# Performance work log

Measured on AMD Instinct MI355X. Metric: run time of the kernel, lower is better.

Reference implementation:

```python
import jax, jax.numpy as jnp
import numpy as np

E = 8          # num_experts
K = 2          # top-k experts per token
CAP_RATIO = 1.05


def setup_inputs() -> dict:
    key = jax.random.key(0)
    ks = jax.random.split(key, 4)
    B, S, D, H = 2, 2048, 1024, 4096
    x = jax.random.normal(ks[0], (B, S, D), jnp.float32)
    Wg = jax.random.normal(ks[1], (E, D), jnp.float32) * 0.02
    W1 = jax.random.normal(ks[2], (E, D, H), jnp.float32) * 0.02
    b1 = jnp.zeros((E, H), jnp.float32)
    W2 = jax.random.normal(ks[3], (E, H, D), jnp.float32) * 0.02
    b2 = jnp.zeros((E, D), jnp.float32)
    return {"x": x, "Wg": Wg, "W1": W1, "b1": b1, "W2": W2, "b2": b2}


def reference(x, Wg, W1, b1, W2, b2):
    # Eval-mode SparseMoE forward (no router noise, no aux-loss metrics).
    B, S, D = x.shape
    T = B * S
    xf = x.reshape(T, D)

    # --- router: softmax gates + top-k ---
    gates = jax.nn.softmax(xf @ Wg.T, axis=-1)          # [T, E]
    topw, topi = jax.lax.top_k(gates, K)                # [T, K]

    # --- capacity-limited dispatch (slot-major order, matching torch loop) ---
    C = int(round(K * T * CAP_RATIO / E))               # buffer capacity per expert
    e_ord = topi.T.reshape(-1)                          # [K*T] expert id per assignment
    tok_ord = jnp.tile(jnp.arange(T), K)                # [K*T] token id per assignment
    oh = jax.nn.one_hot(e_ord, E, dtype=jnp.int32)      # [K*T, E]
    cnt = jnp.take_along_axis(jnp.cumsum(oh, 0) - oh, e_ord[:, None], 1)[:, 0]
    within = cnt < C                                    # first C arrivals per expert accepted
    pos = jnp.where(within, cnt, C)                     # dropped tokens -> dummy slot C

    # scatter accepted tokens into per-expert buffers [E, C+1, D]
    x_disp = xf[tok_ord]
    buf = jnp.zeros((E, C + 1, D), xf.dtype).at[e_ord, pos].add(x_disp)[:, :C]

    # --- grouped expert MLP (Linear -> exact GELU -> Linear) ---
    h = jax.nn.gelu(jnp.einsum('ecd,edh->ech', buf, W1) + b1[:, None, :],
                    approximate=False)
    y = jnp.einsum('ech,ehd->ecd', h, W2) + b2[:, None, :]  # [E, C, D]

    # --- gather back and weighted combine ---
    y_ord = y[e_ord, jnp.minimum(pos, C - 1)] * within[:, None].astype(y.dtype)
    y_tk = y_ord.reshape(K, T, D).transpose(1, 0, 2)     # [T, K, D]
    cw = topw * within.reshape(K, T).T.astype(topw.dtype)
    out = jnp.einsum('tk,tkd->td', cw, y_tk)
    return out.reshape(B, S, D)
```

## Files before the change

### kernel.cpp

```cpp
#include <hip/hip_runtime.h>

typedef __attribute__((ext_vector_type(8))) __bf16 bf16x8;
typedef __attribute__((ext_vector_type(4))) float f32x4;

constexpr int T  = 4096;
constexpr int Dm = 1024;
constexpr int Hm = 4096;
constexpr int NE = 8;
constexpr int CAP = 1075;
constexpr int CP  = 1152;

static __device__ __forceinline__ unsigned short f2bf(float f) {
  unsigned int u = __float_as_uint(f);
  u += 0x7FFFu + ((u >> 16) & 1u);
  return (unsigned short)(u >> 16);
}

static __device__ __forceinline__ void gload_lds16(const void* g, void* l) {
  __builtin_amdgcn_global_load_lds(
      (const __attribute__((address_space(1))) void*)g,
      (__attribute__((address_space(3))) void*)l, 16, 0, 0);
}

__global__ __launch_bounds__(256) void router_kernel(
    const float* __restrict__ x, const float* __restrict__ Wg,
    int* __restrict__ topi, float* __restrict__ topw) {
  int t = blockIdx.x * 4 + (threadIdx.x >> 6);
  int lane = threadIdx.x & 63;
  const float* xr = x + (size_t)t * Dm;
  float acc[NE];
#pragma unroll
  for (int e = 0; e < NE; ++e) acc[e] = 0.f;
  for (int i = lane * 4; i < Dm; i += 256) {
    float4 xv = *(const float4*)(xr + i);
#pragma unroll
    for (int e = 0; e < NE; ++e) {
      float4 wv = *(const float4*)(Wg + e * Dm + i);
      acc[e] += xv.x * wv.x + xv.y * wv.y + xv.z * wv.z + xv.w * wv.w;
    }
  }
#pragma unroll
  for (int off = 32; off > 0; off >>= 1) {
#pragma unroll
    for (int e = 0; e < NE; ++e) acc[e] += __shfl_xor(acc[e], off, 64);
  }
  if (lane == 0) {
    float mx = acc[0];
#pragma unroll
    for (int e = 1; e < NE; ++e) mx = fmaxf(mx, acc[e]);
    float g[NE];
    float s = 0.f;
#pragma unroll
    for (int e = 0; e < NE; ++e) { g[e] = expf(acc[e] - mx); s += g[e]; }
    int i0 = 0; float v0 = g[0];
#pragma unroll
    for (int e = 1; e < NE; ++e) if (g[e] > v0) { v0 = g[e]; i0 = e; }
    int i1 = -1; float v1 = -1e30f;
#pragma unroll
    for (int e = 0; e < NE; ++e) {
      if (e == i0) continue;
      if (g[e] > v1) { v1 = g[e]; i1 = e; }
    }
    float inv = 1.f / s;
    topi[t * 2] = i0; topi[t * 2 + 1] = i1;
    topw[t * 2] = v0 * inv; topw[t * 2 + 1] = v1 * inv;
  }
}

__global__ void dispatch_kernel(const int* __restrict__ topi,
                                int* __restrict__ pos, int* __restrict__ within) {
  int lane = threadIdx.x;
  int cnt[NE];
#pragma unroll
  for (int e = 0; e < NE; ++e) cnt[e] = 0;
  unsigned long long below = (1ULL << lane) - 1ULL;
  for (int c = 0; c < (2 * T) / 64; ++c) {
    int a = c * 64 + lane;
    int k = a >> 12;
    int t = a & (T - 1);
    int e = topi[t * 2 + k];
    int p = 0;
#pragma unroll
    for (int ex = 0; ex < NE; ++ex) {
      unsigned long long m = __ballot(e == ex);
      if (e == ex) p = cnt[ex] + __popcll(m & below);
      cnt[ex] += __popcll(m);
    }
    pos[a] = p;
    within[a] = (p < CAP) ? 1 : 0;
  }
}

__global__ __launch_bounds__(256) void scatter_kernel(
    const float* __restrict__ x, const int* __restrict__ topi,
    const int* __restrict__ pos, const int* __restrict__ within,
    unsigned short* __restrict__ buf) {
  int a = blockIdx.x;
  if (!within[a]) return;
  int k = a >> 12, t = a & (T - 1);
  int e = topi[t * 2 + k];
  int p = pos[a];
  const float* src = x + (size_t)t * Dm;
  unsigned short* dst = buf + ((size_t)e * CP + p) * Dm;
  int i = threadIdx.x * 4;
  float4 v = *(const float4*)(src + i);
  ushort4 o;
  o.x = f2bf(v.x); o.y = f2bf(v.y); o.z = f2bf(v.z); o.w = f2bf(v.w);
  *(ushort4*)(dst + i) = o;
}

__global__ __launch_bounds__(256) void transpose_kernel(
    const float* __restrict__ W, unsigned short* __restrict__ Wt,
    int Kd, int N) {
  __shared__ float tile[64][33];
  const int e = blockIdx.z;
  const int n0 = blockIdx.x * 32;
  const int k0 = blockIdx.y * 64;
  const float* src = W + ((long long)e * Kd + k0) * N + n0;
  const int tid = threadIdx.x;
  const int r = tid >> 3;
  const int c4 = (tid & 7) * 4;
#pragma unroll
  for (int hh = 0; hh < 2; ++hh) {
    float4 v = *(const float4*)(src + (long long)(r + 32 * hh) * N + c4);
    tile[r + 32 * hh][c4] = v.x; tile[r + 32 * hh][c4 + 1] = v.y;
    tile[r + 32 * hh][c4 + 2] = v.z; tile[r + 32 * hh][c4 + 3] = v.w;
  }
  __syncthreads();
  const int n = tid >> 4;
  const int k4 = (tid & 15) * 4;
  unsigned short* dst = Wt + ((long long)e * N + n0) * Kd + k0;
#pragma unroll
  for (int hh = 0; hh < 2; ++hh) {
    int nn = n + 16 * hh;
    ushort4 o;
    o.x = f2bf(tile[k4][nn]);     o.y = f2bf(tile[k4 + 1][nn]);
    o.z = f2bf(tile[k4 + 2][nn]); o.w = f2bf(tile[k4 + 3][nn]);
    *(ushort4*)(dst + (long long)nn * Kd + k4) = o;
  }
}

template <bool GELU, bool OUT_BF16>
__global__ __launch_bounds__(256) void gemm_bt_kernel(
    const unsigned short* __restrict__ Aall, const unsigned short* __restrict__ Btall,
    const float* __restrict__ biasAll, void* __restrict__ OutAll,
    int Kd, int N, long long sA, long long sB, long long sO, int sBias) {
  __shared__ unsigned short Alds[128 * 64];
  __shared__ unsigned short Blds[128 * 64];

  const int e = blockIdx.z;
  const unsigned short* A  = Aall  + (long long)e * sA + (long long)blockIdx.y * 128 * Kd;
  const unsigned short* Bt = Btall + (long long)e * sB + (long long)blockIdx.x * 128 * Kd;
  const float* bias = biasAll + (long long)e * sBias + blockIdx.x * 128;

  const int tid = threadIdx.x;
  const int lane = tid & 63;
  const int wid = tid >> 6;
  const int wr = (wid >> 1) * 64;
  const int wc = (wid & 1) * 64;
  const int l15 = lane & 15;
  const int khi = lane >> 4;
  const int swz = lane & 7;

  const int srow = lane >> 3;
  const int sslot = (lane & 7) ^ srow;

  f32x4 acc[4][4];
#pragma unroll
  for (int m = 0; m < 4; ++m)
#pragma unroll
    for (int n = 0; n < 4; ++n) acc[m][n] = (f32x4){0.f, 0.f, 0.f, 0.f};

  const int nK = Kd >> 6;
  for (int kt = 0; kt < nK; ++kt) {
    const int kb = kt << 6;
#pragma unroll
    for (int j = 0; j < 4; ++j) {
      const int c = wid * 4 + j;
      const long long rowg = 8 * c + srow;
      gload_lds16(A  + rowg * Kd + kb + sslot * 8, &Alds[c * 512]);
      gload_lds16(Bt + rowg * Kd + kb + sslot * 8, &Blds[c * 512]);
    }
    __syncthreads();
#pragma unroll
    for (int kk = 0; kk < 2; ++kk) {
      bf16x8 af[4], bfv[4];
#pragma unroll
      for (int m = 0; m < 4; ++m)
        af[m] = *(const bf16x8*)&Alds[(wr + m * 16 + l15) * 64 + (((kk * 4 + khi) ^ swz) << 3)];
#pragma unroll
      for (int n = 0; n < 4; ++n)
        bfv[n] = *(const bf16x8*)&Blds[(wc + n * 16 + l15) * 64 + (((kk * 4 + khi) ^ swz) << 3)];
#pragma unroll
      for (int m = 0; m < 4; ++m)
#pragma unroll
        for (int n = 0; n < 4; ++n)
          acc[m][n] = __builtin_amdgcn_mfma_f32_16x16x32_bf16(af[m], bfv[n], acc[m][n], 0, 0, 0);
    }
    __syncthreads();
  }

  const int crow = khi * 4;
#pragma unroll
  for (int m = 0; m < 4; ++m) {
#pragma unroll
    for (int n = 0; n < 4; ++n) {
      const long long col = (long long)blockIdx.x * 128 + wc + n * 16 + l15;
      const float bvv = bias[wc + n * 16 + l15];
#pragma unroll
      for (int j = 0; j < 4; ++j) {
        const long long row = (long long)blockIdx.y * 128 + wr + m * 16 + crow + j;
        float v = acc[m][n][j] + bvv;
        if (GELU) v = 0.5f * v * (1.f + erff(v * 0.70710678118654752f));
        if (OUT_BF16)
          ((unsigned short*)OutAll)[(long long)e * sO + row * N + col] = f2bf(v);
        else
          ((float*)OutAll)[(long long)e * sO + row * N + col] = v;
      }
    }
  }
}

__global__ __launch_bounds__(256) void combine_kernel(
    const float* __restrict__ y, const int* __restrict__ topi,
    const float* __restrict__ topw, const int* __restrict__ pos,
    const int* __restrict__ within, float* __restrict__ out) {
  int t = blockIdx.x;
  int i = threadIdx.x * 4;
  float4 r = {0.f, 0.f, 0.f, 0.f};
#pragma unroll
  for (int k = 0; k < 2; ++k) {
    int a = k * T + t;
    if (within[a]) {
      int e = topi[t * 2 + k];
      int p = pos[a];
      float w = topw[t * 2 + k];
      const float* yr = y + ((size_t)e * CP + p) * Dm;
      float4 v = *(const float4*)(yr + i);
      r.x += w * v.x; r.y += w * v.y; r.z += w * v.z; r.w += w * v.w;
    }
  }
  *(float4*)(out + (size_t)t * Dm + i) = r;
}

extern "C" void kernel_launch(void* const* d_in, const int* in_sizes, int n_in,
                              void* d_out, int out_size, void* d_ws, size_t ws_size,
                              hipStream_t stream) {
  const float* x  = (const float*)d_in[0];
  const float* Wg = (const float*)d_in[1];
  const float* W1 = (const float*)d_in[2];
  const float* b1 = (const float*)d_in[3];
  const float* W2 = (const float*)d_in[4];
  const float* b2 = (const float*)d_in[5];
  float* out = (float*)d_out;

  char* ws = (char*)d_ws;
  const size_t sz_h = (size_t)NE * CP * Hm * 2;
  const size_t sz_y = (size_t)NE * CP * Dm * 4;
  const size_t sz_wt_full = (size_t)NE * Hm * Dm * 2;
  const size_t needA = sz_h + sz_y + sz_wt_full + (size_t)2 * T * 16;
  const int EB = (ws_size >= needA) ? NE : 2;

  unsigned short* h = (unsigned short*)ws;
  char* yreg = ws + sz_h;
  unsigned short* buf = (unsigned short*)yreg;
  float* y = (float*)yreg;
  unsigned short* Wt = (unsigned short*)(ws + sz_h + sz_y);
  char* smallp = ws + sz_h + sz_y + (size_t)EB * Hm * Dm * 2;
  int* topi   = (int*)smallp;
  float* topw = (float*)(topi + 2 * T);
  int* pos    = (int*)(topw + 2 * T);
  int* within = pos + 2 * T;

  router_kernel<<<T / 4, 256, 0, stream>>>(x, Wg, topi, topw);
  dispatch_kernel<<<1, 64, 0, stream>>>(topi, pos, within);
  scatter_kernel<<<2 * T, 256, 0, stream>>>(x, topi, pos, within, buf);

  for (int e0 = 0; e0 < NE; e0 += EB) {
    transpose_kernel<<<dim3(Hm / 32, Dm / 64, EB), 256, 0, stream>>>(
        W1 + (size_t)e0 * Dm * Hm, Wt, Dm, Hm);
    gemm_bt_kernel<true, true><<<dim3(Hm / 128, CP / 128, EB), 256, 0, stream>>>(
        buf + (size_t)e0 * CP * Dm, Wt, b1 + (size_t)e0 * Hm,
        (void*)(h + (size_t)e0 * CP * Hm),
        Dm, Hm, (long long)CP * Dm, (long long)Hm * Dm, (long long)CP * Hm, Hm);
  }
  for (int e0 = 0; e0 < NE; e0 += EB) {
    transpose_kernel<<<dim3(Dm / 32, Hm / 64, EB), 256, 0, stream>>>(
        W2 + (size_t)e0 * Hm * Dm, Wt, Hm, Dm);
    gemm_bt_kernel<false, false><<<dim3(Dm / 128, CP / 128, EB), 256, 0, stream>>>(
        h + (size_t)e0 * CP * Hm, Wt, b2 + (size_t)e0 * Dm,
        (void*)(y + (size_t)e0 * CP * Dm),
        Hm, Dm, (long long)CP * Hm, (long long)Dm * Hm, (long long)CP * Dm, Dm);
  }

  combine_kernel<<<T, 256, 0, stream>>>(y, topi, topw, pos, within, out);
}
```

Measured before the change: 397.6 us.

## Parallelize dispatch with block-wide packed scan and remap GEMM grid to 1D

```diff
diff --git a/kernel.cpp b/kernel.cpp
--- a/kernel.cpp
+++ b/kernel.cpp
@@ -67,25 +67,43 @@
   }
 }
 
-__global__ void dispatch_kernel(const int* __restrict__ topi,
-                                int* __restrict__ pos, int* __restrict__ within) {
-  int lane = threadIdx.x;
-  int cnt[NE];
-#pragma unroll
-  for (int e = 0; e < NE; ++e) cnt[e] = 0;
-  unsigned long long below = (1ULL << lane) - 1ULL;
-  for (int c = 0; c < (2 * T) / 64; ++c) {
-    int a = c * 64 + lane;
+__global__ __launch_bounds__(1024) void dispatch_scan_kernel(
+    const int* __restrict__ topi, int* __restrict__ pos, int* __restrict__ within) {
+  __shared__ unsigned long long sc0[1024];
+  __shared__ unsigned long long sc1[1024];
+  const int tid = threadIdx.x;
+  int myE[8];
+  unsigned long long w0 = 0, w1 = 0;
+#pragma unroll
+  for (int j = 0; j < 8; ++j) {
+    int a = tid * 8 + j;
     int k = a >> 12;
     int t = a & (T - 1);
     int e = topi[t * 2 + k];
-    int p = 0;
-#pragma unroll
-    for (int ex = 0; ex < NE; ++ex) {
-      unsigned long long m = __ballot(e == ex);
-      if (e == ex) p = cnt[ex] + __popcll(m & below);
-      cnt[ex] += __popcll(m);
-    }
+    myE[j] = e;
+    unsigned long long inc = 1ULL << (16 * (e & 3));
+    if (e < 4) w0 += inc; else w1 += inc;
+  }
+  const unsigned long long l0 = w0, l1 = w1;
+  sc0[tid] = w0; sc1[tid] = w1;
+  __syncthreads();
+  for (int off = 1; off < 1024; off <<= 1) {
+    unsigned long long a0 = 0, a1 = 0;
+    if (tid >= off) { a0 = sc0[tid - off]; a1 = sc1[tid - off]; }
+    __syncthreads();
+    w0 += a0; w1 += a1;
+    sc0[tid] = w0; sc1[tid] = w1;
+    __syncthreads();
+  }
+  unsigned long long e0 = w0 - l0, e1 = w1 - l1;
+#pragma unroll
+  for (int j = 0; j < 8; ++j) {
+    int a = tid * 8 + j;
+    int e = myE[j];
+    int sh = 16 * (e & 3);
+    int p;
+    if (e < 4) { p = (int)((e0 >> sh) & 0xFFFF); e0 += 1ULL << sh; }
+    else       { p = (int)((e1 >> sh) & 0xFFFF); e1 += 1ULL << sh; }
     pos[a] = p;
     within[a] = (p < CAP) ? 1 : 0;
   }
@@ -144,14 +162,20 @@
 __global__ __launch_bounds__(256) void gemm_bt_kernel(
     const unsigned short* __restrict__ Aall, const unsigned short* __restrict__ Btall,
     const float* __restrict__ biasAll, void* __restrict__ OutAll,
-    int Kd, int N, long long sA, long long sB, long long sO, int sBias) {
+    int Kd, int N, long long sA, long long sB, long long sO, int sBias,
+    int eb, int nM) {
   __shared__ unsigned short Alds[128 * 64];
   __shared__ unsigned short Blds[128 * 64];
 
-  const int e = blockIdx.z;
-  const unsigned short* A  = Aall  + (long long)e * sA + (long long)blockIdx.y * 128 * Kd;
-  const unsigned short* Bt = Btall + (long long)e * sB + (long long)blockIdx.x * 128 * Kd;
-  const float* bias = biasAll + (long long)e * sBias + blockIdx.x * 128;
+  const int lin = blockIdx.x;
+  const int e = lin % eb;
+  const int q = lin / eb;
+  const int mb = q % nM;
+  const int nb = q / nM;
+
+  const unsigned short* A  = Aall  + (long long)e * sA + (long long)mb * 128 * Kd;
+  const unsigned short* Bt = Btall + (long long)e * sB + (long long)nb * 128 * Kd;
+  const float* bias = biasAll + (long long)e * sBias + nb * 128;
 
   const int tid = threadIdx.x;
   const int lane = tid & 63;
@@ -205,11 +229,11 @@
   for (int m = 0; m < 4; ++m) {
 #pragma unroll
     for (int n = 0; n < 4; ++n) {
-      const long long col = (long long)blockIdx.x * 128 + wc + n * 16 + l15;
+      const long long col = (long long)nb * 128 + wc + n * 16 + l15;
       const float bvv = bias[wc + n * 16 + l15];
 #pragma unroll
       for (int j = 0; j < 4; ++j) {
-        const long long row = (long long)blockIdx.y * 128 + wr + m * 16 + crow + j;
+        const long long row = (long long)mb * 128 + wr + m * 16 + crow + j;
         float v = acc[m][n][j] + bvv;
         if (GELU) v = 0.5f * v * (1.f + erff(v * 0.70710678118654752f));
         if (OUT_BF16)
@@ -273,24 +297,27 @@
   int* within = pos + 2 * T;
 
   router_kernel<<<T / 4, 256, 0, stream>>>(x, Wg, topi, topw);
-  dispatch_kernel<<<1, 64, 0, stream>>>(topi, pos, within);
+  dispatch_scan_kernel<<<1, 1024, 0, stream>>>(topi, pos, within);
   scatter_kernel<<<2 * T, 256, 0, stream>>>(x, topi, pos, within, buf);
 
+  const int nM = CP / 128;
   for (int e0 = 0; e0 < NE; e0 += EB) {
     transpose_kernel<<<dim3(Hm / 32, Dm / 64, EB), 256, 0, stream>>>(
         W1 + (size_t)e0 * Dm * Hm, Wt, Dm, Hm);
-    gemm_bt_kernel<true, true><<<dim3(Hm / 128, CP / 128, EB), 256, 0, stream>>>(
+    gemm_bt_kernel<true, true><<<EB * nM * (Hm / 128), 256, 0, stream>>>(
         buf + (size_t)e0 * CP * Dm, Wt, b1 + (size_t)e0 * Hm,
         (void*)(h + (size_t)e0 * CP * Hm),
-        Dm, Hm, (long long)CP * Dm, (long long)Hm * Dm, (long long)CP * Hm, Hm);
+        Dm, Hm, (long long)CP * Dm, (long long)Hm * Dm, (long long)CP * Hm, Hm,
+        EB, nM);
   }
   for (int e0 = 0; e0 < NE; e0 += EB) {
     transpose_kernel<<<dim3(Dm / 32, Hm / 64, EB), 256, 0, stream>>>(
         W2 + (size_t)e0 * Hm * Dm, Wt, Hm, Dm);
-    gemm_bt_kernel<false, false><<<dim3(Dm / 128, CP / 128, EB), 256, 0, stream>>>(
+    gemm_bt_kernel<false, false><<<EB * nM * (Dm / 128), 256, 0, stream>>>(
         h + (size_t)e0 * CP * Hm, Wt, b2 + (size_t)e0 * Dm,
         (void*)(y + (size_t)e0 * CP * Dm),
-        Hm, Dm, (long long)CP * Hm, (long long)Dm * Hm, (long long)CP * Dm, Dm);
+        Hm, Dm, (long long)CP * Hm, (long long)Dm * Hm, (long long)CP * Dm, Dm,
+        EB, nM);
   }
 
   combine_kernel<<<T, 256, 0, stream>>>(y, topi, topw, pos, within, out);
```

Measured after the change: 344.1 us. -13.4%, faster.
